# Kernel tuning notes

Measured on AMD Instinct MI355X. Metric: run time of the kernel, lower is better.

The kernel has to match this reference:

```python
import jax, jax.numpy as jnp
import numpy as np

EPS = 0.01  # eigenvalue cutoff in vstars_from_quadrics


def _cluster(predicted_points, samples, normals):
    # predicted_points: [B,M,3]; samples, normals: [B,N,3]
    B, N, _ = samples.shape
    M = predicted_points.shape[1]

    # --- knn_points with k=1: argmin_m ||s_n - p_m||^2 = argmin_m (|p_m|^2 - 2 s.p) ---
    dots = jnp.einsum('bnd,bmd->bnm', samples, predicted_points)      # [B,N,M]
    pp2 = jnp.sum(predicted_points * predicted_points, axis=-1)       # [B,M]
    closest_idx = jnp.argmin(pp2[:, None, :] - 2.0 * dots, axis=-1)   # [B,N] int

    # --- per-sample plane quadric (ps ps^T), ps = [n, -n.s] ---
    ds = -jnp.sum(normals * samples, axis=-1)                          # [B,N]
    ps = jnp.concatenate([normals, ds[..., None]], axis=-1)            # [B,N,4]
    quadrics = (ps[..., :, None] * ps[..., None, :]).reshape(B, N, 16)  # [B,N,16]

    # --- scatter_mean into M voronoi bins (zero default for empty bins) ---
    seg_sum = jax.vmap(lambda v, i: jax.ops.segment_sum(v, i, num_segments=M))
    q_sum = seg_sum(quadrics, closest_idx)                              # [B,M,16]
    n_sum = seg_sum(normals, closest_idx)                               # [B,M,3]
    cnt = seg_sum(jnp.ones((B, N, 1), quadrics.dtype), closest_idx)     # [B,M,1]
    denom = jnp.maximum(cnt, 1.0)
    target_quadrics = (q_sum / denom).reshape(B, M, 4, 4)
    mean_normals = n_sum / denom

    non_void = jnp.sum(mean_normals * mean_normals, axis=-1) > 0        # [B,M] bool

    # --- vstars_from_quadrics (computed densely, masked where bin is empty) ---
    A = target_quadrics[..., :3, :3]                                    # [B,M,3,3]
    bvec = -target_quadrics[..., 3, :3]                                 # [B,M,3]
    # void bins -> A == 0; substitute a well-conditioned matrix so SVD is safe,
    # result is masked to 0 anyway (rhs is 0 there as well).
    fake = jnp.diag(jnp.asarray([3.0, 2.0, 1.0], A.dtype))
    A_safe = jnp.where(non_void[..., None, None], A, fake)
    u, eigs, vh = jnp.linalg.svd(A_safe)                                # eigs desc
    ratio = eigs / jnp.maximum(eigs[..., 0:1], 1e-20)
    mask_s = ratio > EPS
    eigs2 = jnp.where(mask_s, 1.0 / jnp.where(mask_s, eigs, 1.0), 0.0)  # [B,M,3]
    rhs = bvec - jnp.einsum('bmij,bmj->bmi', A, predicted_points)       # b - A p
    t = jnp.einsum('bmji,bmj->bmi', u, rhs)                             # U^T rhs
    delta = jnp.einsum('bmji,bmj->bmi', vh, eigs2 * t)                  # Vh^T D U^T rhs
    vstars = predicted_points + delta
    vstars = jnp.where(non_void[..., None], vstars, 0.0)
    return A, mean_normals, vstars, non_void


def setup_inputs() -> dict:
    key = jax.random.key(0)
    k1, k2, k3 = jax.random.split(key, 3)
    B, M, N = 4, 1024, 65536
    predicted_points = jax.random.normal(k1, (B, M, 3), dtype=jnp.float32)
    samples = jax.random.normal(k2, (B, N, 3), dtype=jnp.float32)
    normals = jax.random.normal(k3, (B, N, 3), dtype=jnp.float32)
    normals = normals / jnp.linalg.norm(normals, axis=-1, keepdims=True)
    return {"predicted_points": predicted_points, "samples": samples, "normals": normals}


def reference(predicted_points, samples, normals):
    target_As, mean_normals, vstars, non_void = _cluster(predicted_points, samples, normals)
    return target_As, mean_normals, vstars, non_void
```

## Files before the change

kernel.cpp:

```cpp
#include <hip/hip_runtime.h>

#define BB 4
#define MM 1024
#define NN 65536
#define CL (BB * MM)

__global__ __launch_bounds__(256) void k_clear(int4* __restrict__ head4)
{
    head4[blockIdx.x * 256 + threadIdx.x] = make_int4(-1, -1, -1, -1);
}

__global__ __launch_bounds__(512) void k_assign(
    const float* __restrict__ pp, const float* __restrict__ smp,
    int* __restrict__ head, int* __restrict__ next)
{
    __shared__ float4 pts[MM];
    __shared__ float bestSh[8][256];
    __shared__ int   biSh[8][256];

    const int b   = blockIdx.x >> 8;
    const int blk = blockIdx.x & 255;
    const float* P = pp + b * MM * 3;
    for (int i = threadIdx.x; i < MM; i += 512) {
        float x = P[i * 3 + 0], y = P[i * 3 + 1], z = P[i * 3 + 2];
        pts[i] = make_float4(x, y, z, x * x + y * y + z * z);
    }
    __syncthreads();

    const int l  = threadIdx.x & 63;
    const int g  = threadIdx.x >> 6;
    const int nb = blk * 256;
    const float* S = smp + (size_t)b * NN * 3;

    float ax[4], ay[4], az[4], best[4];
    int bi[4];
#pragma unroll
    for (int j = 0; j < 4; ++j) {
        int n = nb + j * 64 + l;
        ax[j] = -2.0f * S[n * 3 + 0];
        ay[j] = -2.0f * S[n * 3 + 1];
        az[j] = -2.0f * S[n * 3 + 2];
        best[j] = 3.4e38f;
        bi[j] = 0;
    }
    const int m0 = g * 128;
#pragma unroll 4
    for (int mi = 0; mi < 128; ++mi) {
        float4 p = pts[m0 + mi];
#pragma unroll
        for (int j = 0; j < 4; ++j) {
            float sc = fmaf(ax[j], p.x, fmaf(ay[j], p.y, fmaf(az[j], p.z, p.w)));
            if (sc < best[j]) { best[j] = sc; bi[j] = m0 + mi; }
        }
    }
#pragma unroll
    for (int j = 0; j < 4; ++j) {
        bestSh[g][j * 64 + l] = best[j];
        biSh[g][j * 64 + l]   = bi[j];
    }
    __syncthreads();

    if (threadIdx.x < 256) {
        const int t = threadIdx.x;
        float bb = bestSh[0][t];
        int   ii = biSh[0][t];
#pragma unroll
        for (int gg = 1; gg < 8; ++gg) {
            float bo = bestSh[gg][t];
            int   io = biSh[gg][t];
            if (bo < bb) { bb = bo; ii = io; }
        }
        const int n = nb + t;
        const int gc = b * MM + ii;
        next[(size_t)b * NN + n] = atomicExch(&head[gc * 64 + (t & 63)], n);
    }
}


#define ROTJ(APP, AQQ, APQ, ARP, ARQ, V0P, V1P, V2P, V0Q, V1Q, V2Q)            \
    do {                                                                       \
        double apq_ = APQ;                                                     \
        if (fabs(apq_) > 1e-300) {                                             \
            double theta_ = (AQQ - APP) / (2.0 * apq_);                        \
            double t_ = 1.0 / (fabs(theta_) + sqrt(theta_ * theta_ + 1.0));    \
            if (theta_ < 0.0) t_ = -t_;                                        \
            double c_ = 1.0 / sqrt(t_ * t_ + 1.0), sn_ = t_ * c_;              \
            APP -= t_ * apq_; AQQ += t_ * apq_; APQ = 0.0;                     \
            double arp_ = ARP, arq_ = ARQ;                                     \
            ARP = c_ * arp_ - sn_ * arq_;                                      \
            ARQ = sn_ * arp_ + c_ * arq_;                                      \
            double x_;                                                         \
            x_ = V0P; V0P = c_ * x_ - sn_ * V0Q; V0Q = sn_ * x_ + c_ * V0Q;    \
            x_ = V1P; V1P = c_ * x_ - sn_ * V1Q; V1Q = sn_ * x_ + c_ * V1Q;    \
            x_ = V2P; V2P = c_ * x_ - sn_ * V2Q; V2Q = sn_ * x_ + c_ * V2Q;    \
        }                                                                      \
    } while (0)

#define CESWAP(EI, EJ, VA, VB, VC, WA, WB, WC)                                 \
    do {                                                                       \
        if (EI < EJ) {                                                         \
            double tt_;                                                        \
            tt_ = EI; EI = EJ; EJ = tt_;                                       \
            tt_ = VA; VA = WA; WA = tt_;                                       \
            tt_ = VB; VB = WB; WB = tt_;                                       \
            tt_ = VC; VC = WC; WC = tt_;                                       \
        }                                                                      \
    } while (0)

__global__ __launch_bounds__(256) void k_cluster(
    const float* __restrict__ pp, const float* __restrict__ smp,
    const float* __restrict__ nrm, const int* __restrict__ head,
    const int* __restrict__ next, float* __restrict__ out)
{
    const int wave = blockIdx.x * 4 + (threadIdx.x >> 6);
    const int lane = threadIdx.x & 63;
    const int b = wave >> 10;
    const int* NX = next + (size_t)b * NN;
    const float* S  = smp + (size_t)b * NN * 3;
    const float* Nr = nrm + (size_t)b * NN * 3;

    double q00 = 0, q01 = 0, q02 = 0, q11 = 0, q12 = 0, q22 = 0;
    double nd0 = 0, nd1 = 0, nd2 = 0, s0 = 0, s1 = 0, s2 = 0;
    int count = 0;

    int cur = head[wave * 64 + lane];
    while (cur >= 0) {
        double sxv = S[cur * 3 + 0], syv = S[cur * 3 + 1], szv = S[cur * 3 + 2];
        double nx = Nr[cur * 3 + 0], ny = Nr[cur * 3 + 1], nz = Nr[cur * 3 + 2];
        double d = -(nx * sxv + ny * syv + nz * szv);
        q00 += nx * nx; q01 += nx * ny; q02 += nx * nz;
        q11 += ny * ny; q12 += ny * nz; q22 += nz * nz;
        nd0 += nx * d; nd1 += ny * d; nd2 += nz * d;
        s0 += nx; s1 += ny; s2 += nz;
        ++count;
        cur = NX[cur];
    }
#pragma unroll
    for (int o = 32; o > 0; o >>= 1) {
        q00 += __shfl_xor(q00, o); q01 += __shfl_xor(q01, o); q02 += __shfl_xor(q02, o);
        q11 += __shfl_xor(q11, o); q12 += __shfl_xor(q12, o); q22 += __shfl_xor(q22, o);
        nd0 += __shfl_xor(nd0, o); nd1 += __shfl_xor(nd1, o); nd2 += __shfl_xor(nd2, o);
        s0  += __shfl_xor(s0, o);  s1  += __shfl_xor(s1, o);  s2  += __shfl_xor(s2, o);
        count += __shfl_xor(count, o);
    }

    double denom = count > 1 ? (double)count : 1.0;
    double A00 = q00 / denom, A01 = q01 / denom, A02 = q02 / denom;
    double A11 = q11 / denom, A12 = q12 / denom, A22 = q22 / denom;
    double mn0 = s0 / denom, mn1 = s1 / denom, mn2 = s2 / denom;
    double bv0 = -nd0 / denom, bv1 = -nd1 / denom, bv2 = -nd2 / denom;
    bool nonvoid = (mn0 * mn0 + mn1 * mn1 + mn2 * mn2) > 0.0;

    double vs0 = 0, vs1 = 0, vs2 = 0;
    if (nonvoid) {
        double a00 = A00, a01 = A01, a02 = A02, a11 = A11, a12 = A12, a22 = A22;
        double v00 = 1, v01 = 0, v02 = 0;
        double v10 = 0, v11 = 1, v12 = 0;
        double v20 = 0, v21 = 0, v22 = 1;
#pragma unroll
        for (int sweep = 0; sweep < 8; ++sweep) {
            ROTJ(a00, a11, a01, a02, a12, v00, v10, v20, v01, v11, v21);
            ROTJ(a00, a22, a02, a01, a12, v00, v10, v20, v02, v12, v22);
            ROTJ(a11, a22, a12, a01, a02, v01, v11, v21, v02, v12, v22);
        }
        double e0 = a00, e1 = a11, e2 = a22;
        CESWAP(e0, e1, v00, v10, v20, v01, v11, v21);
        CESWAP(e0, e2, v00, v10, v20, v02, v12, v22);
        CESWAP(e1, e2, v01, v11, v21, v02, v12, v22);

        double emax = e0 > 1e-20 ? e0 : 1e-20;
        const float* Pp = pp + (size_t)wave * 3;
        double px = Pp[0], py = Pp[1], pz = Pp[2];
        double r0 = bv0 - (A00 * px + A01 * py + A02 * pz);
        double r1 = bv1 - (A01 * px + A11 * py + A12 * pz);
        double r2 = bv2 - (A02 * px + A12 * py + A22 * pz);
        double thr = 0.01 * emax;
        if (e0 > thr) { double w = (v00 * r0 + v10 * r1 + v20 * r2) / e0; vs0 += w * v00; vs1 += w * v10; vs2 += w * v20; }
        if (e1 > thr) { double w = (v01 * r0 + v11 * r1 + v21 * r2) / e1; vs0 += w * v01; vs1 += w * v11; vs2 += w * v21; }
        if (e2 > thr) { double w = (v02 * r0 + v12 * r1 + v22 * r2) / e2; vs0 += w * v02; vs1 += w * v12; vs2 += w * v22; }
        vs0 += px; vs1 += py; vs2 += pz;
    }

    if (lane == 0) {
        float* Ao = out + (size_t)wave * 9;
        Ao[0] = (float)A00; Ao[1] = (float)A01; Ao[2] = (float)A02;
        Ao[3] = (float)A01; Ao[4] = (float)A11; Ao[5] = (float)A12;
        Ao[6] = (float)A02; Ao[7] = (float)A12; Ao[8] = (float)A22;
        float* Mo = out + 36864 + (size_t)wave * 3;
        Mo[0] = (float)mn0; Mo[1] = (float)mn1; Mo[2] = (float)mn2;
        float* Vo = out + 49152 + (size_t)wave * 3;
        Vo[0] = (float)vs0; Vo[1] = (float)vs1; Vo[2] = (float)vs2;
        out[61440 + wave] = nonvoid ? 1.0f : 0.0f;
    }
}

extern "C" void kernel_launch(void* const* d_in, const int* in_sizes, int n_in,
                              void* d_out, int out_size, void* d_ws, size_t ws_size,
                              hipStream_t stream)
{
    const float* pp  = (const float*)d_in[0];
    const float* smp = (const float*)d_in[1];
    const float* nrm = (const float*)d_in[2];
    float* out = (float*)d_out;

    int* head = (int*)d_ws;
    int* next = head + CL * 64;

    k_clear<<<256, 256, 0, stream>>>((int4*)head);
    k_assign<<<1024, 512, 0, stream>>>(pp, smp, head, next);
    k_cluster<<<CL / 4, 256, 0, stream>>>(pp, smp, nrm, head, next, out);
}
```

Baseline: 71.31 us.

## Fuse clear, assign and cluster into one cooperative kernel with grid syncs

Replaces the three separate launches with a single cooperative kernel of 512 blocks that clears the head lists, runs nearest-point assignment over two halves per block, then accumulates and solves clusters after grid-wide barriers. This is meant to remove the per-launch overhead and inter-kernel gaps. The old three-kernel path stays as a fallback if the occupancy query or cooperative launch fails. The cost is two grid syncs and fewer blocks doing twice the assignment work each, and the cluster phase now runs 8 waves per block instead of 4, which changes its occupancy.

```diff
diff --git a/kernel.cpp b/kernel.cpp
--- a/kernel.cpp
+++ b/kernel.cpp
@@ -1,81 +1,12 @@
 #include <hip/hip_runtime.h>
+#include <hip/hip_cooperative_groups.h>
+
+namespace cg = cooperative_groups;
 
 #define BB 4
 #define MM 1024
 #define NN 65536
 #define CL (BB * MM)
-
-__global__ __launch_bounds__(256) void k_clear(int4* __restrict__ head4)
-{
-    head4[blockIdx.x * 256 + threadIdx.x] = make_int4(-1, -1, -1, -1);
-}
-
-__global__ __launch_bounds__(512) void k_assign(
-    const float* __restrict__ pp, const float* __restrict__ smp,
-    int* __restrict__ head, int* __restrict__ next)
-{
-    __shared__ float4 pts[MM];
-    __shared__ float bestSh[8][256];
-    __shared__ int   biSh[8][256];
-
-    const int b   = blockIdx.x >> 8;
-    const int blk = blockIdx.x & 255;
-    const float* P = pp + b * MM * 3;
-    for (int i = threadIdx.x; i < MM; i += 512) {
-        float x = P[i * 3 + 0], y = P[i * 3 + 1], z = P[i * 3 + 2];
-        pts[i] = make_float4(x, y, z, x * x + y * y + z * z);
-    }
-    __syncthreads();
-
-    const int l  = threadIdx.x & 63;
-    const int g  = threadIdx.x >> 6;
-    const int nb = blk * 256;
-    const float* S = smp + (size_t)b * NN * 3;
-
-    float ax[4], ay[4], az[4], best[4];
-    int bi[4];
-#pragma unroll
-    for (int j = 0; j < 4; ++j) {
-        int n = nb + j * 64 + l;
-        ax[j] = -2.0f * S[n * 3 + 0];
-        ay[j] = -2.0f * S[n * 3 + 1];
-        az[j] = -2.0f * S[n * 3 + 2];
-        best[j] = 3.4e38f;
-        bi[j] = 0;
-    }
-    const int m0 = g * 128;
-#pragma unroll 4
-    for (int mi = 0; mi < 128; ++mi) {
-        float4 p = pts[m0 + mi];
-#pragma unroll
-        for (int j = 0; j < 4; ++j) {
-            float sc = fmaf(ax[j], p.x, fmaf(ay[j], p.y, fmaf(az[j], p.z, p.w)));
-            if (sc < best[j]) { best[j] = sc; bi[j] = m0 + mi; }
-        }
-    }
-#pragma unroll
-    for (int j = 0; j < 4; ++j) {
-        bestSh[g][j * 64 + l] = best[j];
-        biSh[g][j * 64 + l]   = bi[j];
-    }
-    __syncthreads();
-
-    if (threadIdx.x < 256) {
-        const int t = threadIdx.x;
-        float bb = bestSh[0][t];
-        int   ii = biSh[0][t];
-#pragma unroll
-        for (int gg = 1; gg < 8; ++gg) {
-            float bo = bestSh[gg][t];
-            int   io = biSh[gg][t];
-            if (bo < bb) { bb = bo; ii = io; }
-        }
-        const int n = nb + t;
-        const int gc = b * MM + ii;
-        next[(size_t)b * NN + n] = atomicExch(&head[gc * 64 + (t & 63)], n);
-    }
-}
-
 
 #define ROTJ(APP, AQQ, APQ, ARP, ARQ, V0P, V1P, V2P, V0Q, V1Q, V2Q)            \
     do {                                                                       \
@@ -107,17 +38,16 @@
         }                                                                      \
     } while (0)
 
-__global__ __launch_bounds__(256) void k_cluster(
-    const float* __restrict__ pp, const float* __restrict__ smp,
-    const float* __restrict__ nrm, const int* __restrict__ head,
-    const int* __restrict__ next, float* __restrict__ out)
-{
-    const int wave = blockIdx.x * 4 + (threadIdx.x >> 6);
-    const int lane = threadIdx.x & 63;
-    const int b = wave >> 10;
-    const int* NX = next + (size_t)b * NN;
-    const float* S  = smp + (size_t)b * NN * 3;
-    const float* Nr = nrm + (size_t)b * NN * 3;
+__device__ __forceinline__ void cluster_body(
+    int wave, int lane, const float* __restrict__ pp,
+    const float* __restrict__ smp, const float* __restrict__ nrm,
+    const int* __restrict__ head, const int* __restrict__ next,
+    float* __restrict__ out)
+{
+    const int bc = wave >> 10;
+    const int* NX = next + (size_t)bc * NN;
+    const float* Sc = smp + (size_t)bc * NN * 3;
+    const float* Nr = nrm + (size_t)bc * NN * 3;
 
     double q00 = 0, q01 = 0, q02 = 0, q11 = 0, q12 = 0, q22 = 0;
     double nd0 = 0, nd1 = 0, nd2 = 0, s0 = 0, s1 = 0, s2 = 0;
@@ -125,7 +55,7 @@
 
     int cur = head[wave * 64 + lane];
     while (cur >= 0) {
-        double sxv = S[cur * 3 + 0], syv = S[cur * 3 + 1], szv = S[cur * 3 + 2];
+        double sxv = Sc[cur * 3 + 0], syv = Sc[cur * 3 + 1], szv = Sc[cur * 3 + 2];
         double nx = Nr[cur * 3 + 0], ny = Nr[cur * 3 + 1], nz = Nr[cur * 3 + 2];
         double d = -(nx * sxv + ny * syv + nz * szv);
         q00 += nx * nx; q01 += nx * ny; q02 += nx * nz;
@@ -194,6 +124,163 @@
     }
 }
 
+__global__ __launch_bounds__(512, 4) void k_fused(
+    const float* __restrict__ pp, const float* __restrict__ smp,
+    const float* __restrict__ nrm, int* __restrict__ head,
+    int* __restrict__ next, float* __restrict__ out)
+{
+    cg::grid_group grid = cg::this_grid();
+
+    __shared__ float4 pts[MM];
+    __shared__ float bestSh[8][256];
+    __shared__ int   biSh[8][256];
+
+    head[blockIdx.x * 512 + threadIdx.x] = -1;
+    const int b   = blockIdx.x >> 7;
+    const int blk = blockIdx.x & 127;
+    const float* P = pp + b * MM * 3;
+    for (int i = threadIdx.x; i < MM; i += 512) {
+        float x = P[i * 3 + 0], y = P[i * 3 + 1], z = P[i * 3 + 2];
+        pts[i] = make_float4(x, y, z, x * x + y * y + z * z);
+    }
+    grid.sync();
+
+    const int l = threadIdx.x & 63;
+    const int g = threadIdx.x >> 6;
+    const float* S = smp + (size_t)b * NN * 3;
+
+    for (int half = 0; half < 2; ++half) {
+        const int nb = blk * 512 + half * 256;
+        float ax[4], ay[4], az[4], best[4];
+        int bi[4];
+#pragma unroll
+        for (int j = 0; j < 4; ++j) {
+            int n = nb + j * 64 + l;
+            ax[j] = -2.0f * S[n * 3 + 0];
+            ay[j] = -2.0f * S[n * 3 + 1];
+            az[j] = -2.0f * S[n * 3 + 2];
+            best[j] = 3.4e38f;
+            bi[j] = 0;
+        }
+        const int m0 = g * 128;
+#pragma unroll 4
+        for (int mi = 0; mi < 128; ++mi) {
+            float4 p = pts[m0 + mi];
+#pragma unroll
+            for (int j = 0; j < 4; ++j) {
+                float sc = fmaf(ax[j], p.x, fmaf(ay[j], p.y, fmaf(az[j], p.z, p.w)));
+                if (sc < best[j]) { best[j] = sc; bi[j] = m0 + mi; }
+            }
+        }
+#pragma unroll
+        for (int j = 0; j < 4; ++j) {
+            bestSh[g][j * 64 + l] = best[j];
+            biSh[g][j * 64 + l]   = bi[j];
+        }
+        __syncthreads();
+
+        if (threadIdx.x < 256) {
+            const int t = threadIdx.x;
+            float bb = bestSh[0][t];
+            int   ii = biSh[0][t];
+#pragma unroll
+            for (int gg = 1; gg < 8; ++gg) {
+                float bo = bestSh[gg][t];
+                int   io = biSh[gg][t];
+                if (bo < bb) { bb = bo; ii = io; }
+            }
+            const int n = nb + t;
+            const int gc = b * MM + ii;
+            next[(size_t)b * NN + n] = atomicExch(&head[gc * 64 + (t & 63)], n);
+        }
+        __syncthreads();
+    }
+    __threadfence();
+    grid.sync();
+
+    cluster_body(blockIdx.x * 8 + g, l, pp, smp, nrm, head, next, out);
+}
+
+__global__ __launch_bounds__(256) void k_clear(int4* __restrict__ head4)
+{
+    head4[blockIdx.x * 256 + threadIdx.x] = make_int4(-1, -1, -1, -1);
+}
+
+__global__ __launch_bounds__(512) void k_assign(
+    const float* __restrict__ pp, const float* __restrict__ smp,
+    int* __restrict__ head, int* __restrict__ next)
+{
+    __shared__ float4 pts[MM];
+    __shared__ float bestSh[8][256];
+    __shared__ int   biSh[8][256];
+
+    const int b   = blockIdx.x >> 8;
+    const int blk = blockIdx.x & 255;
+    const float* P = pp + b * MM * 3;
+    for (int i = threadIdx.x; i < MM; i += 512) {
+        float x = P[i * 3 + 0], y = P[i * 3 + 1], z = P[i * 3 + 2];
+        pts[i] = make_float4(x, y, z, x * x + y * y + z * z);
+    }
+    __syncthreads();
+
+    const int l  = threadIdx.x & 63;
+    const int g  = threadIdx.x >> 6;
+    const int nb = blk * 256;
+    const float* S = smp + (size_t)b * NN * 3;
+
+    float ax[4], ay[4], az[4], best[4];
+    int bi[4];
+#pragma unroll
+    for (int j = 0; j < 4; ++j) {
+        int n = nb + j * 64 + l;
+        ax[j] = -2.0f * S[n * 3 + 0];
+        ay[j] = -2.0f * S[n * 3 + 1];
+        az[j] = -2.0f * S[n * 3 + 2];
+        best[j] = 3.4e38f;
+        bi[j] = 0;
+    }
+    const int m0 = g * 128;
+#pragma unroll 4
+    for (int mi = 0; mi < 128; ++mi) {
+        float4 p = pts[m0 + mi];
+#pragma unroll
+        for (int j = 0; j < 4; ++j) {
+            float sc = fmaf(ax[j], p.x, fmaf(ay[j], p.y, fmaf(az[j], p.z, p.w)));
+            if (sc < best[j]) { best[j] = sc; bi[j] = m0 + mi; }
+        }
+    }
+#pragma unroll
+    for (int j = 0; j < 4; ++j) {
+        bestSh[g][j * 64 + l] = best[j];
+        biSh[g][j * 64 + l]   = bi[j];
+    }
+    __syncthreads();
+
+    if (threadIdx.x < 256) {
+        const int t = threadIdx.x;
+        float bb = bestSh[0][t];
+        int   ii = biSh[0][t];
+#pragma unroll
+        for (int gg = 1; gg < 8; ++gg) {
+            float bo = bestSh[gg][t];
+            int   io = biSh[gg][t];
+            if (bo < bb) { bb = bo; ii = io; }
+        }
+        const int n = nb + t;
+        const int gc = b * MM + ii;
+        next[(size_t)b * NN + n] = atomicExch(&head[gc * 64 + (t & 63)], n);
+    }
+}
+
+__global__ __launch_bounds__(256) void k_cluster(
+    const float* __restrict__ pp, const float* __restrict__ smp,
+    const float* __restrict__ nrm, const int* __restrict__ head,
+    const int* __restrict__ next, float* __restrict__ out)
+{
+    cluster_body(blockIdx.x * 4 + (threadIdx.x >> 6), threadIdx.x & 63,
+                 pp, smp, nrm, head, next, out);
+}
+
 extern "C" void kernel_launch(void* const* d_in, const int* in_sizes, int n_in,
                               void* d_out, int out_size, void* d_ws, size_t ws_size,
                               hipStream_t stream)
@@ -206,6 +293,16 @@
     int* head = (int*)d_ws;
     int* next = head + CL * 64;
 
+    int maxB = 0;
+    hipError_t qe = hipOccupancyMaxActiveBlocksPerMultiprocessor(&maxB, k_fused, 512, 0);
+    if (qe == hipSuccess && maxB >= 2) {
+        void* args[] = { (void*)&pp, (void*)&smp, (void*)&nrm,
+                         (void*)&head, (void*)&next, (void*)&out };
+        hipError_t le = hipLaunchCooperativeKernel((const void*)k_fused,
+                                                   dim3(512), dim3(512),
+                                                   args, 0, stream);
+        if (le == hipSuccess) return;
+    }
     k_clear<<<256, 256, 0, stream>>>((int4*)head);
     k_assign<<<1024, 512, 0, stream>>>(pp, smp, head, next);
     k_cluster<<<CL / 4, 256, 0, stream>>>(pp, smp, nrm, head, next, out);
```

Result: no change. 71.80 us (+0.7%).
